# Optimization experiments

Hardware: AMD Instinct MI355X
Metric: run time of the kernel (lower is better)

Reference implementation:

```python
import jax, jax.numpy as jnp
import numpy as np

N = 50000
E = 800000
IN_DIM = 128
HID = 128


def setup_inputs() -> dict:
    key = jax.random.key(0)
    ks = jax.random.split(key, 8)
    x = jax.random.normal(ks[0], (N, IN_DIM), dtype=jnp.float32)
    edge_index = jax.random.randint(ks[1], (2, E), 0, N, dtype=jnp.int64)
    s1 = 1.0 / np.sqrt(IN_DIM)
    s2 = 1.0 / np.sqrt(HID)
    Wl1 = jax.random.uniform(ks[2], (HID, IN_DIM), jnp.float32, -s1, s1)
    bl1 = jnp.zeros((HID,), jnp.float32)
    Wr1 = jax.random.uniform(ks[3], (HID, IN_DIM), jnp.float32, -s1, s1)
    Wl2 = jax.random.uniform(ks[4], (HID, HID), jnp.float32, -s2, s2)
    bl2 = jnp.zeros((HID,), jnp.float32)
    Wr2 = jax.random.uniform(ks[5], (HID, HID), jnp.float32, -s2, s2)
    return {"x": x, "Wl1": Wl1, "bl1": bl1, "Wr1": Wr1,
            "Wl2": Wl2, "bl2": bl2, "Wr2": Wr2, "edge_index": edge_index}


def _sage_layer(h, src, dst, deg_inv, Wl, bl, Wr):
    # mean aggregation over in-edges: gather source feats, scatter-sum to targets
    msg_sum = jax.ops.segment_sum(h[src], dst, num_segments=N)  # [N, d]
    agg = msg_sum * deg_inv[:, None]
    return agg @ Wl.T + bl + h @ Wr.T


def reference(x, Wl1, bl1, Wr1, Wl2, bl2, Wr2, edge_index):
    src, dst = edge_index[0], edge_index[1]
    deg = jax.ops.segment_sum(jnp.ones((E,), x.dtype), dst, num_segments=N)
    deg_inv = 1.0 / jnp.maximum(deg, 1.0)
    h = jax.nn.relu(_sage_layer(x, src, dst, deg_inv, Wl1, bl1, Wr1))
    h = jax.nn.relu(_sage_layer(h, src, dst, deg_inv, Wl2, bl2, Wr2))
    return h  # dropout is identity in eval mode
```

## Files before the change

kernel.cpp:

```cpp
#include <hip/hip_runtime.h>

#define N_NODES 50000
#define N_ROWS_PAD 50064
#define N_EDGES 800000
#define DIM 128
#define KCAT 256
#define CAP 64
#define MPITCH 264

#define PACK_N (2 * DIM * KCAT)
#define CAST_N (N_NODES * 16)
#define PREP_TOTAL (PACK_N + CAST_N + N_EDGES)

typedef unsigned int u32;
typedef unsigned short u16;
typedef __attribute__((ext_vector_type(8))) short short8;
typedef __attribute__((ext_vector_type(4))) float f32x4;

static __device__ __forceinline__ u16 f2bf(float f) {
  union { float f; u32 u; } v; v.f = f;
  u32 r = v.u + 0x7fffu + ((v.u >> 16) & 1u);
  return (u16)(r >> 16);
}
static __device__ __forceinline__ float bflo(u32 p) { return __uint_as_float(p << 16); }
static __device__ __forceinline__ float bfhi(u32 p) { return __uint_as_float(p & 0xffff0000u); }

__global__ void prep(const float* __restrict__ wl1, const float* __restrict__ wr1,
                     const float* __restrict__ wl2, const float* __restrict__ wr2,
                     const float* __restrict__ x,
                     const int* __restrict__ src, const int* __restrict__ dst,
                     int* __restrict__ cnt, u16* __restrict__ csr,
                     u16* __restrict__ wcat, u32* __restrict__ bufx) {
  int idx = blockIdx.x * blockDim.x + threadIdx.x;
  if (idx < PACK_N) {
    int layer = idx >> 15;
    int n = (idx >> 8) & 127;
    int k = idx & 255;
    const float* wl = layer ? wl2 : wl1;
    const float* wr = layer ? wr2 : wr1;
    float v = (k < DIM) ? wl[n * DIM + k] : wr[n * DIM + (k - DIM)];
    wcat[idx] = f2bf(v);
  } else if (idx < PACK_N + CAST_N) {
    int t = idx - PACK_N;
    int node = t >> 4, q = t & 15;
    float4 v0 = ((const float4*)x)[(size_t)node * 32 + q * 2];
    float4 v1 = ((const float4*)x)[(size_t)node * 32 + q * 2 + 1];
    uint4 p;
    p.x = (u32)f2bf(v0.x) | ((u32)f2bf(v0.y) << 16);
    p.y = (u32)f2bf(v0.z) | ((u32)f2bf(v0.w) << 16);
    p.z = (u32)f2bf(v1.x) | ((u32)f2bf(v1.y) << 16);
    p.w = (u32)f2bf(v1.z) | ((u32)f2bf(v1.w) << 16);
    ((uint4*)bufx)[(size_t)node * 16 + q] = p;
  } else {
    int e = idx - (PACK_N + CAST_N);
    if (e < N_EDGES) {
      int d = dst[e];
      int pos = atomicAdd(&cnt[d], 1);
      if (pos < CAP)
        __builtin_nontemporal_store((u16)src[e], &csr[(size_t)pos * N_NODES + d]);
    }
  }
}

__global__ __launch_bounds__(256) void fused_layer(
    const u16* __restrict__ hin, const u16* __restrict__ csr,
    const int* __restrict__ cnt, const u16* __restrict__ wcat,
    const float* __restrict__ bias, float* __restrict__ fout,
    u16* __restrict__ bout) {
  __shared__ u16 smsg[4 * 16 * MPITCH];
  const int lane = threadIdx.x & 63;
  const int wv = threadIdx.x >> 6;
  const int row0 = blockIdx.x * 64 + wv * 16;
  const int sub = lane >> 4, q = lane & 15;
  const uint4* h16 = (const uint4*)hin;
  u16* msgw = smsg + wv * 16 * MPITCH;

  for (int r = 0; r < 16; ++r) {
    int node = row0 + r;
    if (node >= N_NODES) break;
    int craw = cnt[node];
    int c = min(craw, CAP);
    const u16* col = csr + node;
    float a0 = 0, a1 = 0, a2 = 0, a3 = 0, a4 = 0, a5 = 0, a6 = 0, a7 = 0;
#define ACC8(u) { a0 += bflo(u.x); a1 += bfhi(u.x); a2 += bflo(u.y); a3 += bfhi(u.y); \
                  a4 += bflo(u.z); a5 += bfhi(u.z); a6 += bflo(u.w); a7 += bfhi(u.w); }
    int i = sub;
    for (; i + 12 < c; i += 16) {
      u32 s0 = col[(size_t)i * N_NODES];
      u32 s1 = col[(size_t)(i + 4) * N_NODES];
      u32 s2 = col[(size_t)(i + 8) * N_NODES];
      u32 s3 = col[(size_t)(i + 12) * N_NODES];
      uint4 u0 = h16[(size_t)s0 * 16 + q];
      uint4 u1 = h16[(size_t)s1 * 16 + q];
      uint4 u2 = h16[(size_t)s2 * 16 + q];
      uint4 u3 = h16[(size_t)s3 * 16 + q];
      ACC8(u0); ACC8(u1); ACC8(u2); ACC8(u3);
    }
    for (; i < c; i += 4) {
      uint4 u0 = h16[(size_t)((u32)col[(size_t)i * N_NODES]) * 16 + q];
      ACC8(u0);
    }
#undef ACC8
    a0 += __shfl_xor(a0, 16); a1 += __shfl_xor(a1, 16);
    a2 += __shfl_xor(a2, 16); a3 += __shfl_xor(a3, 16);
    a4 += __shfl_xor(a4, 16); a5 += __shfl_xor(a5, 16);
    a6 += __shfl_xor(a6, 16); a7 += __shfl_xor(a7, 16);
    a0 += __shfl_xor(a0, 32); a1 += __shfl_xor(a1, 32);
    a2 += __shfl_xor(a2, 32); a3 += __shfl_xor(a3, 32);
    a4 += __shfl_xor(a4, 32); a5 += __shfl_xor(a5, 32);
    a6 += __shfl_xor(a6, 32); a7 += __shfl_xor(a7, 32);
    if (lane < 16) {
      float di = 1.0f / (float)max(craw, 1);
      uint4 p;
      p.x = (u32)f2bf(a0 * di) | ((u32)f2bf(a1 * di) << 16);
      p.y = (u32)f2bf(a2 * di) | ((u32)f2bf(a3 * di) << 16);
      p.z = (u32)f2bf(a4 * di) | ((u32)f2bf(a5 * di) << 16);
      p.w = (u32)f2bf(a6 * di) | ((u32)f2bf(a7 * di) << 16);
      *(uint4*)&msgw[r * MPITCH + q * 8] = p;
    }
  }
  __syncthreads();

  const int l15 = lane & 15;
  const int ch = lane >> 4;
  const short8* bp = (const short8*)(wcat + (size_t)l15 * KCAT + ch * 8);

  f32x4 acc[8];
#pragma unroll
  for (int t = 0; t < 8; ++t) acc[t] = (f32x4){0.f, 0.f, 0.f, 0.f};

#pragma unroll
  for (int ks = 0; ks < 4; ++ks) {
    short8 a = *(const short8*)&msgw[l15 * MPITCH + ch * 8 + ks * 32];
#pragma unroll
    for (int nt = 0; nt < 8; ++nt)
      acc[nt] = __builtin_amdgcn_mfma_f32_16x16x32_bf16(a, bp[nt * 512 + ks * 4],
                                                        acc[nt], 0, 0, 0);
  }
  const short8* ap = (const short8*)(hin + (size_t)(row0 + l15) * DIM + ch * 8);
#pragma unroll
  for (int ks = 0; ks < 4; ++ks) {
    short8 a = ap[ks * 4];
#pragma unroll
    for (int nt = 0; nt < 8; ++nt)
      acc[nt] = __builtin_amdgcn_mfma_f32_16x16x32_bf16(
          a, bp[nt * 512 + (4 + ks) * 4], acc[nt], 0, 0, 0);
  }

  const int rbase = row0 + (ch << 2);
#pragma unroll
  for (int nt = 0; nt < 8; ++nt) {
    int colj = nt * 16 + l15;
    float bb = bias[colj];
#pragma unroll
    for (int r = 0; r < 4; ++r) {
      int row = rbase + r;
      if (row < N_NODES) {
        float v = fmaxf(acc[nt][r] + bb, 0.f);
        if (fout) fout[(size_t)row * DIM + colj] = v;
        if (bout) bout[(size_t)row * DIM + colj] = f2bf(v);
      }
    }
  }
}

extern "C" void kernel_launch(void* const* d_in, const int* in_sizes, int n_in,
                              void* d_out, int out_size, void* d_ws, size_t ws_size,
                              hipStream_t stream) {
  const float* x   = (const float*)d_in[0];
  const float* Wl1 = (const float*)d_in[1];
  const float* bl1 = (const float*)d_in[2];
  const float* Wr1 = (const float*)d_in[3];
  const float* Wl2 = (const float*)d_in[4];
  const float* bl2 = (const float*)d_in[5];
  const float* Wr2 = (const float*)d_in[6];
  const int* eidx  = (const int*)d_in[7];
  const int* src = eidx;
  const int* dst = eidx + N_EDGES;
  float* out = (float*)d_out;

  char* ws = (char*)d_ws;
  int* cnt  = (int*)ws;
  u16* csr  = (u16*)(ws + 256 * 1024);
  u16* wcat = (u16*)(ws + 6815744);
  u16* bufx = (u16*)(ws + 6946816);
  u16* bufh = (u16*)(ws + 19763200);

  hipMemsetAsync(cnt, 0, N_NODES * sizeof(int), stream);

  prep<<<PREP_TOTAL / 256, 256, 0, stream>>>(Wl1, Wr1, Wl2, Wr2, x, src, dst,
                                             cnt, csr, wcat, (u32*)bufx);

  const int grid = N_ROWS_PAD / 64;

  fused_layer<<<grid, 256, 0, stream>>>(bufx, csr, cnt, wcat, bl1,
                                        (float*)nullptr, bufh);
  fused_layer<<<grid, 256, 0, stream>>>(bufh, csr, cnt, wcat + DIM * KCAT, bl2,
                                        out, (u16*)nullptr);
}
```

Baseline: 320.3 us.

## Shrink block to 16 rows, split rows and output columns across waves

```diff
diff --git a/kernel.cpp b/kernel.cpp
--- a/kernel.cpp
+++ b/kernel.cpp
@@ -67,16 +67,15 @@
     const int* __restrict__ cnt, const u16* __restrict__ wcat,
     const float* __restrict__ bias, float* __restrict__ fout,
     u16* __restrict__ bout) {
-  __shared__ u16 smsg[4 * 16 * MPITCH];
+  __shared__ u16 smsg[16 * MPITCH];
   const int lane = threadIdx.x & 63;
   const int wv = threadIdx.x >> 6;
-  const int row0 = blockIdx.x * 64 + wv * 16;
+  const int row0 = blockIdx.x * 16;
   const int sub = lane >> 4, q = lane & 15;
   const uint4* h16 = (const uint4*)hin;
-  u16* msgw = smsg + wv * 16 * MPITCH;
-
-  for (int r = 0; r < 16; ++r) {
-    int node = row0 + r;
+
+  for (int r = 0; r < 4; ++r) {
+    int node = row0 + wv * 4 + r;
     if (node >= N_NODES) break;
     int craw = cnt[node];
     int c = min(craw, CAP);
@@ -116,7 +115,7 @@
       p.y = (u32)f2bf(a2 * di) | ((u32)f2bf(a3 * di) << 16);
       p.z = (u32)f2bf(a4 * di) | ((u32)f2bf(a5 * di) << 16);
       p.w = (u32)f2bf(a6 * di) | ((u32)f2bf(a7 * di) << 16);
-      *(uint4*)&msgw[r * MPITCH + q * 8] = p;
+      *(uint4*)&smsg[(wv * 4 + r) * MPITCH + q * 8] = p;
     }
   }
   __syncthreads();
@@ -125,38 +124,42 @@
   const int ch = lane >> 4;
   const short8* bp = (const short8*)(wcat + (size_t)l15 * KCAT + ch * 8);
 
-  f32x4 acc[8];
-#pragma unroll
-  for (int t = 0; t < 8; ++t) acc[t] = (f32x4){0.f, 0.f, 0.f, 0.f};
+  f32x4 acc[2];
+  acc[0] = (f32x4){0.f, 0.f, 0.f, 0.f};
+  acc[1] = (f32x4){0.f, 0.f, 0.f, 0.f};
 
 #pragma unroll
   for (int ks = 0; ks < 4; ++ks) {
-    short8 a = *(const short8*)&msgw[l15 * MPITCH + ch * 8 + ks * 32];
-#pragma unroll
-    for (int nt = 0; nt < 8; ++nt)
-      acc[nt] = __builtin_amdgcn_mfma_f32_16x16x32_bf16(a, bp[nt * 512 + ks * 4],
-                                                        acc[nt], 0, 0, 0);
+    short8 a = *(const short8*)&smsg[l15 * MPITCH + ch * 8 + ks * 32];
+#pragma unroll
+    for (int t = 0; t < 2; ++t) {
+      int nt = wv * 2 + t;
+      acc[t] = __builtin_amdgcn_mfma_f32_16x16x32_bf16(a, bp[nt * 512 + ks * 4],
+                                                       acc[t], 0, 0, 0);
+    }
   }
   const short8* ap = (const short8*)(hin + (size_t)(row0 + l15) * DIM + ch * 8);
 #pragma unroll
   for (int ks = 0; ks < 4; ++ks) {
     short8 a = ap[ks * 4];
 #pragma unroll
-    for (int nt = 0; nt < 8; ++nt)
-      acc[nt] = __builtin_amdgcn_mfma_f32_16x16x32_bf16(
-          a, bp[nt * 512 + (4 + ks) * 4], acc[nt], 0, 0, 0);
+    for (int t = 0; t < 2; ++t) {
+      int nt = wv * 2 + t;
+      acc[t] = __builtin_amdgcn_mfma_f32_16x16x32_bf16(
+          a, bp[nt * 512 + (4 + ks) * 4], acc[t], 0, 0, 0);
+    }
   }
 
   const int rbase = row0 + (ch << 2);
 #pragma unroll
-  for (int nt = 0; nt < 8; ++nt) {
-    int colj = nt * 16 + l15;
+  for (int t = 0; t < 2; ++t) {
+    int colj = (wv * 2 + t) * 16 + l15;
     float bb = bias[colj];
 #pragma unroll
     for (int r = 0; r < 4; ++r) {
       int row = rbase + r;
       if (row < N_NODES) {
-        float v = fmaxf(acc[nt][r] + bb, 0.f);
+        float v = fmaxf(acc[t][r] + bb, 0.f);
         if (fout) fout[(size_t)row * DIM + colj] = v;
         if (bout) bout[(size_t)row * DIM + colj] = f2bf(v);
       }
@@ -191,7 +194,7 @@
   prep<<<PREP_TOTAL / 256, 256, 0, stream>>>(Wl1, Wr1, Wl2, Wr2, x, src, dst,
                                              cnt, csr, wcat, (u32*)bufx);
 
-  const int grid = N_ROWS_PAD / 64;
+  const int grid = N_ROWS_PAD / 16;
 
   fused_layer<<<grid, 256, 0, stream>>>(bufx, csr, cnt, wcat, bl1,
                                         (float*)nullptr, bufh);
```

Result: faster. 278.8 us (-12.9%).
